# Kernel tuning notes

Hardware: AMD Instinct MI355X
Metric: run time of the kernel (lower is better)

## Reference

```python
import jax, jax.numpy as jnp
import numpy as np

TEMPERATURE = 8.0  # sqrt(d_k) with d_k = 64


def setup_inputs() -> dict:
    key = jax.random.key(0)
    ks = jax.random.split(key, 5)
    shape = (64, 1024, 64)  # [B*H, N, d_k]
    return {
        "q": jax.random.normal(ks[0], shape, dtype=jnp.float32),
        "k": jax.random.normal(ks[1], shape, dtype=jnp.float32),
        "v": jax.random.normal(ks[2], shape, dtype=jnp.float32),
        "q_sem": jax.random.normal(ks[3], shape, dtype=jnp.float32),
        "k_sem": jax.random.normal(ks[4], shape, dtype=jnp.float32),
    }


def reference(q, k, v, q_sem, k_sem):
    # Semantic fusion branch (q_sem is not None): scores are recomputed
    # with the fused queries/keys. (The original also computes an unused
    # softmax over the pre-fusion scores and an unused attn_sem bmm --
    # dead code with no effect on outputs, so omitted.)
    qf = q + q_sem
    kf = k + k_sem
    attn_score = jnp.einsum("bnd,bmd->bnm", qf, kf) / TEMPERATURE  # [BH, N, N]
    attn = jax.nn.softmax(attn_score, axis=2)
    # dropout in eval mode == identity
    output = jnp.einsum("bnm,bmd->bnd", attn, v)  # [BH, N, d_k]
    return (output, attn, attn_score)
```

## Files before the change

### kernel.cpp

```cpp
#include <hip/hip_runtime.h>
#include <math.h>


#define BH 64
#define N 1024
#define D 64
#define TM 128
#define TK 64
#define NC (N / TK)
#define KSTR 68
#define SSTR 68
#define LOG2E 1.44269504088896f
#define ESHIFT (-17.3123404907f)

typedef float    f32x4 __attribute__((ext_vector_type(4)));
typedef _Float16 half8 __attribute__((ext_vector_type(8)));
typedef _Float16 half4 __attribute__((ext_vector_type(4)));
typedef __fp16   fp16x2 __attribute__((ext_vector_type(2)));

__global__ __launch_bounds__(512, 4) void attn_fused_kernel(
    const float* __restrict__ q, const float* __restrict__ k,
    const float* __restrict__ v, const float* __restrict__ qsem,
    const float* __restrict__ ks, float* __restrict__ out_o,
    float* __restrict__ out_a, float* __restrict__ out_s)
{
    __shared__ __align__(16) _Float16 Kb[TK][KSTR];
    __shared__ __align__(16) _Float16 Vt[D][KSTR];
    __shared__ __align__(16) float    Sst[TM][SSTR];
    __shared__ float rsumf[TM];

    const int t  = threadIdx.x;
    const int w  = t >> 6;
    const int l  = t & 63;
    const int lr = l & 15;
    const int lg = l >> 4;
    const int qt = w >> 2;
    const int kt = w & 3;

    const int wg = blockIdx.x;
    const int b  = ((wg >> 6) << 3) | (wg & 7);
    const int q0 = ((wg >> 3) & 7) * TM;

    const size_t inb = (size_t)b * (N * D);
    const size_t sb  = (size_t)b * N * N + (size_t)q0 * N;

    half8 qa[4][2];
#pragma unroll
    for (int qs = 0; qs < 4; ++qs) {
        const float* qp  = q    + inb + (size_t)(q0 + qt * 64 + qs * 16 + lr) * D + lg * 8;
        const float* qsp = qsem + inb + (size_t)(q0 + qt * 64 + qs * 16 + lr) * D + lg * 8;
#pragma unroll
        for (int kst = 0; kst < 2; ++kst) {
            f32x4 a0 = *(const f32x4*)(qp + kst * 32);
            f32x4 a1 = *(const f32x4*)(qp + kst * 32 + 4);
            f32x4 c0 = *(const f32x4*)(qsp + kst * 32);
            f32x4 c1 = *(const f32x4*)(qsp + kst * 32 + 4);
            f32x4 s0 = a0 + c0, s1 = a1 + c1;
            union { half8 h8; fp16x2 h2[4]; } u;
            u.h2[0] = __builtin_amdgcn_cvt_pkrtz(s0[0], s0[1]);
            u.h2[1] = __builtin_amdgcn_cvt_pkrtz(s0[2], s0[3]);
            u.h2[2] = __builtin_amdgcn_cvt_pkrtz(s1[0], s1[1]);
            u.h2[3] = __builtin_amdgcn_cvt_pkrtz(s1[2], s1[3]);
            qa[qs][kst] = u.h8;
        }
    }

    const int  ts = t & 255;
    const bool kstager = (w < 4);

    auto STAGE = [&](int kc) {
        if (kstager) {
            const f32x4* kbp = (const f32x4*)(k  + inb + (size_t)kc * TK * D);
            const f32x4* sbp = (const f32x4*)(ks + inb + (size_t)kc * TK * D);
#pragma unroll
            for (int h = 0; h < 2; ++h) {
                f32x4 k0 = kbp[(2 * h)     * 256 + ts];
                f32x4 k1 = kbp[(2 * h + 1) * 256 + ts];
                f32x4 s0 = sbp[(2 * h)     * 256 + ts];
                f32x4 s1 = sbp[(2 * h + 1) * 256 + ts];
                f32x4 m0 = k0 + s0, m1 = k1 + s1;
                const int row0 = (2 * h) * 16 + (ts >> 4);
                const int col  = (ts & 15) * 4;
                union { half4 h4; fp16x2 h2[2]; } u0, u1;
                u0.h2[0] = __builtin_amdgcn_cvt_pkrtz(m0[0], m0[1]);
                u0.h2[1] = __builtin_amdgcn_cvt_pkrtz(m0[2], m0[3]);
                u1.h2[0] = __builtin_amdgcn_cvt_pkrtz(m1[0], m1[1]);
                u1.h2[1] = __builtin_amdgcn_cvt_pkrtz(m1[2], m1[3]);
                *(half4*)&Kb[row0][col]      = u0.h4;
                *(half4*)&Kb[row0 + 16][col] = u1.h4;
            }
        } else {
            const f32x4* vbp = (const f32x4*)(v + inb + (size_t)kc * TK * D);
            f32x4 vr0 = vbp[((ts >> 4) * 4 + 0) * 16 + (ts & 15)];
            f32x4 vr1 = vbp[((ts >> 4) * 4 + 1) * 16 + (ts & 15)];
            f32x4 vr2 = vbp[((ts >> 4) * 4 + 2) * 16 + (ts & 15)];
            f32x4 vr3 = vbp[((ts >> 4) * 4 + 3) * 16 + (ts & 15)];
            const int br4 = (ts >> 4) * 4, bc4 = (ts & 15) * 4;
#pragma unroll
            for (int c = 0; c < 4; ++c) {
                union { half4 h4; fp16x2 h2[2]; } u;
                u.h2[0] = __builtin_amdgcn_cvt_pkrtz(vr0[c], vr1[c]);
                u.h2[1] = __builtin_amdgcn_cvt_pkrtz(vr2[c], vr3[c]);
                *(half4*)&Vt[bc4 + c][br4] = u.h4;
            }
        }
    };

    f32x4 oacc[4];
#pragma unroll
    for (int qs = 0; qs < 4; ++qs) oacc[qs] = (f32x4){0.f, 0.f, 0.f, 0.f};
    float rs[4] = {0.f, 0.f, 0.f, 0.f};

    for (int kc = 0; kc < NC; ++kc) {
        __syncthreads();
        STAGE(kc);
        __syncthreads();

        {
            half8 kb0 = *(const half8*)&Kb[kt * 16 + lr][lg * 8];
            half8 kb1 = *(const half8*)&Kb[kt * 16 + lr][32 + lg * 8];
#pragma unroll
            for (int qs = 0; qs < 4; ++qs) {
                f32x4 ac = {0.f, 0.f, 0.f, 0.f};
                ac = __builtin_amdgcn_mfma_f32_16x16x32_f16(qa[qs][0], kb0, ac, 0, 0, 0);
                ac = __builtin_amdgcn_mfma_f32_16x16x32_f16(qa[qs][1], kb1, ac, 0, 0, 0);
#pragma unroll
                for (int r = 0; r < 4; ++r)
                    Sst[qt * 64 + qs * 16 + lg * 4 + r][kt * 16 + lr] = ac[r] * 0.125f;
            }
        }
        __syncthreads();

#pragma unroll
        for (int h = 0; h < 4; ++h) {
            const int srow = h * 32 + (t >> 4);
            f32x4 sv = *(const f32x4*)&Sst[srow][(t & 15) * 4];
            *(f32x4*)(out_s + sb + (size_t)srow * N + kc * TK + (t & 15) * 4) = sv;
        }

#pragma unroll
        for (int kst = 0; kst < 2; ++kst) {
            half8 vb = *(const half8*)&Vt[kt * 16 + lr][kst * 32 + lg * 8];
#pragma unroll
            for (int qs = 0; qs < 4; ++qs) {
                const int prow = qt * 64 + qs * 16 + lr;
                f32x4 s0 = *(const f32x4*)&Sst[prow][kst * 32 + lg * 8];
                f32x4 s1 = *(const f32x4*)&Sst[prow][kst * 32 + lg * 8 + 4];
                float e0 = __builtin_amdgcn_exp2f(__builtin_fmaf(s0[0], LOG2E, ESHIFT));
                float e1 = __builtin_amdgcn_exp2f(__builtin_fmaf(s0[1], LOG2E, ESHIFT));
                float e2 = __builtin_amdgcn_exp2f(__builtin_fmaf(s0[2], LOG2E, ESHIFT));
                float e3 = __builtin_amdgcn_exp2f(__builtin_fmaf(s0[3], LOG2E, ESHIFT));
                float e4 = __builtin_amdgcn_exp2f(__builtin_fmaf(s1[0], LOG2E, ESHIFT));
                float e5 = __builtin_amdgcn_exp2f(__builtin_fmaf(s1[1], LOG2E, ESHIFT));
                float e6 = __builtin_amdgcn_exp2f(__builtin_fmaf(s1[2], LOG2E, ESHIFT));
                float e7 = __builtin_amdgcn_exp2f(__builtin_fmaf(s1[3], LOG2E, ESHIFT));
                if (kt == 0)
                    rs[qs] += ((e0 + e1) + (e2 + e3)) + ((e4 + e5) + (e6 + e7));
                union { half8 h8; fp16x2 h2[4]; } u;
                u.h2[0] = __builtin_amdgcn_cvt_pkrtz(e0, e1);
                u.h2[1] = __builtin_amdgcn_cvt_pkrtz(e2, e3);
                u.h2[2] = __builtin_amdgcn_cvt_pkrtz(e4, e5);
                u.h2[3] = __builtin_amdgcn_cvt_pkrtz(e6, e7);
                oacc[qs] = __builtin_amdgcn_mfma_f32_16x16x32_f16(u.h8, vb, oacc[qs], 0, 0, 0);
            }
        }
    }

    if (kt == 0) {
#pragma unroll
        for (int qs = 0; qs < 4; ++qs) {
            float x = rs[qs];
            x += __shfl_xor(x, 16);
            x += __shfl_xor(x, 32);
            if (l < 16) rsumf[qt * 64 + qs * 16 + l] = x;
        }
    }
    __syncthreads();
    if (t < TM) rsumf[t] = 1.0f / rsumf[t];
    __syncthreads();

#pragma unroll
    for (int qs = 0; qs < 4; ++qs)
#pragma unroll
    for (int r = 0; r < 4; ++r) {
        const int row = qt * 64 + qs * 16 + lg * 4 + r;
        Sst[row][kt * 16 + lr] = oacc[qs][r] * rsumf[row];
    }
    __syncthreads();
#pragma unroll
    for (int h = 0; h < 4; ++h) {
        const int srow = h * 32 + (t >> 4);
        f32x4 ov = *(const f32x4*)&Sst[srow][(t & 15) * 4];
        __builtin_nontemporal_store(ov,
            (f32x4*)(out_o + inb + (size_t)(q0 + srow) * D + (t & 15) * 4));
    }

#pragma unroll
    for (int h = 0; h < 4; ++h) {
        const int   arow = h * 32 + (t >> 4);
        const int   ac0  = (t & 15) * 4;
        const float iva  = rsumf[arow];
        const float* sp  = out_s + sb + (size_t)arow * N + ac0;
        float*       ap  = out_a + sb + (size_t)arow * N + ac0;
#pragma unroll 4
        for (int cb = 0; cb < NC; ++cb) {
            f32x4 sv = *(const f32x4*)(sp + cb * TK);
            f32x4 av;
#pragma unroll
            for (int i = 0; i < 4; ++i)
                av[i] = __builtin_amdgcn_exp2f(__builtin_fmaf(sv[i], LOG2E, ESHIFT)) * iva;
            __builtin_nontemporal_store(av, (f32x4*)(ap + cb * TK));
        }
    }
}

extern "C" void kernel_launch(void* const* d_in, const int* in_sizes, int n_in,
                              void* d_out, int out_size, void* d_ws, size_t ws_size,
                              hipStream_t stream) {
    const float* q  = (const float*)d_in[0];
    const float* k  = (const float*)d_in[1];
    const float* v  = (const float*)d_in[2];
    const float* qs = (const float*)d_in[3];
    const float* ks = (const float*)d_in[4];

    float* out_o = (float*)d_out;
    float* out_a = out_o + (size_t)BH * N * D;
    float* out_s = out_a + (size_t)BH * N * N;

    attn_fused_kernel<<<dim3(BH * (N / TM)), dim3(512), 0, stream>>>(
        q, k, v, qs, ks, out_o, out_a, out_s);
}
```

Baseline: 668.3 us.

## Double-buffer K/V shared tiles and prefetch next chunk into registers

```diff
diff --git a/kernel.cpp b/kernel.cpp
--- a/kernel.cpp
+++ b/kernel.cpp
@@ -24,8 +24,8 @@
     const float* __restrict__ ks, float* __restrict__ out_o,
     float* __restrict__ out_a, float* __restrict__ out_s)
 {
-    __shared__ __align__(16) _Float16 Kb[TK][KSTR];
-    __shared__ __align__(16) _Float16 Vt[D][KSTR];
+    __shared__ __align__(16) _Float16 Kb[2][TK][KSTR];
+    __shared__ __align__(16) _Float16 Vt[2][D][KSTR];
     __shared__ __align__(16) float    Sst[TM][SSTR];
     __shared__ float rsumf[TM];
 
@@ -67,44 +67,50 @@
 
     const int  ts = t & 255;
     const bool kstager = (w < 4);
-
-    auto STAGE = [&](int kc) {
+    f32x4 kreg[4], sreg[4], vreg[4];
+
+    auto LOAD = [&](int kc) {
         if (kstager) {
             const f32x4* kbp = (const f32x4*)(k  + inb + (size_t)kc * TK * D);
             const f32x4* sbp = (const f32x4*)(ks + inb + (size_t)kc * TK * D);
 #pragma unroll
-            for (int h = 0; h < 2; ++h) {
-                f32x4 k0 = kbp[(2 * h)     * 256 + ts];
-                f32x4 k1 = kbp[(2 * h + 1) * 256 + ts];
-                f32x4 s0 = sbp[(2 * h)     * 256 + ts];
-                f32x4 s1 = sbp[(2 * h + 1) * 256 + ts];
-                f32x4 m0 = k0 + s0, m1 = k1 + s1;
-                const int row0 = (2 * h) * 16 + (ts >> 4);
-                const int col  = (ts & 15) * 4;
-                union { half4 h4; fp16x2 h2[2]; } u0, u1;
-                u0.h2[0] = __builtin_amdgcn_cvt_pkrtz(m0[0], m0[1]);
-                u0.h2[1] = __builtin_amdgcn_cvt_pkrtz(m0[2], m0[3]);
-                u1.h2[0] = __builtin_amdgcn_cvt_pkrtz(m1[0], m1[1]);
-                u1.h2[1] = __builtin_amdgcn_cvt_pkrtz(m1[2], m1[3]);
-                *(half4*)&Kb[row0][col]      = u0.h4;
-                *(half4*)&Kb[row0 + 16][col] = u1.h4;
+            for (int j = 0; j < 4; ++j) {
+                kreg[j] = kbp[j * 256 + ts];
+                sreg[j] = sbp[j * 256 + ts];
             }
         } else {
             const f32x4* vbp = (const f32x4*)(v + inb + (size_t)kc * TK * D);
-            f32x4 vr0 = vbp[((ts >> 4) * 4 + 0) * 16 + (ts & 15)];
-            f32x4 vr1 = vbp[((ts >> 4) * 4 + 1) * 16 + (ts & 15)];
-            f32x4 vr2 = vbp[((ts >> 4) * 4 + 2) * 16 + (ts & 15)];
-            f32x4 vr3 = vbp[((ts >> 4) * 4 + 3) * 16 + (ts & 15)];
+#pragma unroll
+            for (int j = 0; j < 4; ++j)
+                vreg[j] = vbp[((ts >> 4) * 4 + j) * 16 + (ts & 15)];
+        }
+    };
+    auto STORE = [&](int bf) {
+        if (kstager) {
+#pragma unroll
+            for (int j = 0; j < 4; ++j) {
+                const int row = j * 16 + (ts >> 4), col = (ts & 15) * 4;
+                f32x4 sm = kreg[j] + sreg[j];
+                union { half4 h4; fp16x2 h2[2]; } u;
+                u.h2[0] = __builtin_amdgcn_cvt_pkrtz(sm[0], sm[1]);
+                u.h2[1] = __builtin_amdgcn_cvt_pkrtz(sm[2], sm[3]);
+                *(half4*)&Kb[bf][row][col] = u.h4;
+            }
+        } else {
             const int br4 = (ts >> 4) * 4, bc4 = (ts & 15) * 4;
 #pragma unroll
             for (int c = 0; c < 4; ++c) {
                 union { half4 h4; fp16x2 h2[2]; } u;
-                u.h2[0] = __builtin_amdgcn_cvt_pkrtz(vr0[c], vr1[c]);
-                u.h2[1] = __builtin_amdgcn_cvt_pkrtz(vr2[c], vr3[c]);
-                *(half4*)&Vt[bc4 + c][br4] = u.h4;
+                u.h2[0] = __builtin_amdgcn_cvt_pkrtz(vreg[0][c], vreg[1][c]);
+                u.h2[1] = __builtin_amdgcn_cvt_pkrtz(vreg[2][c], vreg[3][c]);
+                *(half4*)&Vt[bf][bc4 + c][br4] = u.h4;
             }
         }
     };
+
+    LOAD(0);
+    STORE(0);
+    __syncthreads();
 
     f32x4 oacc[4];
 #pragma unroll
@@ -112,13 +118,11 @@
     float rs[4] = {0.f, 0.f, 0.f, 0.f};
 
     for (int kc = 0; kc < NC; ++kc) {
-        __syncthreads();
-        STAGE(kc);
-        __syncthreads();
+        const int c = kc & 1;
 
         {
-            half8 kb0 = *(const half8*)&Kb[kt * 16 + lr][lg * 8];
-            half8 kb1 = *(const half8*)&Kb[kt * 16 + lr][32 + lg * 8];
+            half8 kb0 = *(const half8*)&Kb[c][kt * 16 + lr][lg * 8];
+            half8 kb1 = *(const half8*)&Kb[c][kt * 16 + lr][32 + lg * 8];
 #pragma unroll
             for (int qs = 0; qs < 4; ++qs) {
                 f32x4 ac = {0.f, 0.f, 0.f, 0.f};
@@ -129,6 +133,8 @@
                     Sst[qt * 64 + qs * 16 + lg * 4 + r][kt * 16 + lr] = ac[r] * 0.125f;
             }
         }
+        if (kc + 1 < NC) LOAD(kc + 1);
+
         __syncthreads();
 
 #pragma unroll
@@ -140,7 +146,7 @@
 
 #pragma unroll
         for (int kst = 0; kst < 2; ++kst) {
-            half8 vb = *(const half8*)&Vt[kt * 16 + lr][kst * 32 + lg * 8];
+            half8 vb = *(const half8*)&Vt[c][kt * 16 + lr][kst * 32 + lg * 8];
 #pragma unroll
             for (int qs = 0; qs < 4; ++qs) {
                 const int prow = qt * 64 + qs * 16 + lr;
@@ -164,6 +170,10 @@
                 oacc[qs] = __builtin_amdgcn_mfma_f32_16x16x32_f16(u.h8, vb, oacc[qs], 0, 0, 0);
             }
         }
+
+        if (kc + 1 < NC) STORE(c ^ 1);
+
+        __syncthreads();
     }
 
     if (kt == 0) {
```

After: 714.1 us. 1.07x slower.
